# Optimization experiments

Hardware: AMD Instinct MI355X
Metric: run time of the kernel (lower is better)

The kernel has to match this reference:

```python
import jax, jax.numpy as jnp
import numpy as np

INPUT_DIM = 2048
NUM_EXPERTS = 64
TOP_K = 8
BATCH = 16384


def setup_inputs() -> dict:
    key = jax.random.key(0)
    k_x, k_n, k_wg, k_bg, k_wn = jax.random.split(key, 5)
    x = jax.random.normal(k_x, (BATCH, INPUT_DIM), dtype=jnp.float32)
    noise = jax.random.normal(k_n, (BATCH, NUM_EXPERTS), dtype=jnp.float32)
    Wg = jax.random.normal(k_wg, (NUM_EXPERTS, INPUT_DIM), dtype=jnp.float32) * 0.02
    bg = jax.random.normal(k_bg, (NUM_EXPERTS,), dtype=jnp.float32) * 0.02
    Wn = jax.random.normal(k_wn, (NUM_EXPERTS, INPUT_DIM), dtype=jnp.float32) * 0.02
    return {"x": x, "noise": noise, "Wg": Wg, "bg": bg, "Wn": Wn}


def reference(x, noise, Wg, bg, Wn):
    # logits: (B, E)
    logits = jnp.einsum("bd,ed->be", x, Wg) + bg
    noise_stddev = jax.nn.softplus(jnp.einsum("bd,ed->be", x, Wn))
    noisy_logits = logits + noise * noise_stddev

    top_k_values, top_k_indices = jax.lax.top_k(noisy_logits, TOP_K)  # (B, K)
    top_k_weights = jax.nn.softmax(top_k_values, axis=-1)

    # aux losses
    dispatch = jnp.argmax(noisy_logits, axis=-1)            # (B,)
    f = jax.nn.one_hot(dispatch, NUM_EXPERTS, dtype=logits.dtype).mean(axis=0)  # (E,)
    p = jax.nn.softmax(logits, axis=-1).mean(axis=0)        # (E,)
    load_balance_loss = NUM_EXPERTS * jnp.sum(f * p)
    z_loss = jnp.mean(jax.nn.logsumexp(logits, axis=-1) ** 2)

    return top_k_weights, top_k_indices, load_balance_loss, z_loss
```

## Files before the change

### kernel.cpp

```cpp
#include <hip/hip_runtime.h>
#include <math.h>

#define IDIM 2048
#define NE   64
#define TOPK 8
#define NB   16384
#define BM   32
#define BK   64
#define NCH  (IDIM / BK)
#define NQ   4
#define KQ   512
#define NCHQ 8
#define TAU  1e-4f

#define WS_CNT 129
#define WS_LIST 130
#define WSPLIT_BYTE 66560
#define WSPLIT_REQ  (WSPLIT_BYTE + NCH * 32768)
#define PART_BYTE   (WSPLIT_BYTE + NCH * 32768)
#define SPLIT_REQ   (PART_BYTE + (size_t)NQ * NB * 128 * 4)

typedef __attribute__((ext_vector_type(8))) short bf16x8_t;
typedef __attribute__((ext_vector_type(4))) float f32x4_t;

__device__ __forceinline__ float softplusf(float v) {
    return (v > 0.f) ? (v + log1pf(expf(-v))) : log1pf(expf(v));
}
__device__ __forceinline__ double softplus_d(double v) {
    return (v > 0.0) ? (v + log1p(exp(-v))) : log1p(exp(v));
}

__device__ __forceinline__ short f2bf(float f) {
    unsigned u = __float_as_uint(f);
    unsigned r = (u + 0x7FFFu + ((u >> 16) & 1u)) >> 16;
    return (short)r;
}
__device__ __forceinline__ float bf2f(short s) {
    return __uint_as_float(((unsigned)(unsigned short)s) << 16);
}

__global__ void init_ws_kernel(float* ws) {
    int t = threadIdx.x;
    if (t < WS_LIST) ws[t] = 0.0f;
}

__device__ __forceinline__ void split8(const float4 v0, const float4 v1,
                                       bf16x8_t& H, bf16x8_t& L) {
    float fv[8] = {v0.x, v0.y, v0.z, v0.w, v1.x, v1.y, v1.z, v1.w};
    #pragma unroll
    for (int q = 0; q < 8; ++q) {
        short hb = f2bf(fv[q]);
        short lb = f2bf(fv[q] - bf2f(hb));
        H[q] = hb; L[q] = lb;
    }
}

__device__ __forceinline__ void cvt_slot(const float4 v0, const float4 v1,
                                         char* hiP, char* loP, int off) {
    bf16x8_t H, L;
    split8(v0, v1, H, L);
    *(bf16x8_t*)(hiP + off) = H;
    *(bf16x8_t*)(loP + off) = L;
}

__global__ __launch_bounds__(256) void prep_kernel(
    const float* __restrict__ Wg, const float* __restrict__ Wn,
    char* __restrict__ wsW, float* __restrict__ ws)
{
    if (blockIdx.x == 128) {
        if (threadIdx.x < WS_LIST) ws[threadIdx.x] = 0.0f;
        return;
    }
    int g = blockIdx.x * 256 + threadIdx.x;
    int t = g >> 10, i = g & 1023;
    int row = i >> 3, wslot = i & 7;
    int kslot = wslot ^ (row & 7);
    const float* src = (row < 64 ? Wg + (size_t)row * IDIM
                                 : Wn + (size_t)(row - 64) * IDIM) + t * BK + kslot * 8;
    float4 v0 = *(const float4*)src;
    float4 v1 = *(const float4*)(src + 4);
    bf16x8_t H, L;
    split8(v0, v1, H, L);
    char* dst = wsW + (size_t)t * 32768;
    *(bf16x8_t*)(dst + i * 16)         = H;
    *(bf16x8_t*)(dst + 16384 + i * 16) = L;
}

__global__ __launch_bounds__(512, 4) void gemm_quarter_kernel(
    const float* __restrict__ x, const char* __restrict__ wsW,
    float* __restrict__ part)
{
    __shared__ char smem[40960] __attribute__((aligned(16)));
    char* AH = smem;
    char* AL = smem + 4096;
    char* BH = smem + 8192;
    char* BL = smem + 24576;

    const int u   = threadIdx.x;
    const int w   = u >> 6;
    const int l   = u & 63;
    const int lr  = l & 15;
    const int lg4 = l >> 4;
    const int s7  = lr & 7;
    const int q   = blockIdx.x & 3;
    const int row0 = (blockIdx.x >> 2) * BM;
    float* pb = part + (size_t)q * NB * 128;

    const int ar  = (u >> 3) & 31;
    const int ac  = u & 7;
    const int aoff = ar * 128 + (((ac ^ (ar & 7)) & 7) << 4);
    const float* pa = x + (size_t)(row0 + ar) * IDIM + q * KQ + ac * 8;

    f32x4_t acc[2];
    #pragma unroll
    for (int mt = 0; mt < 2; ++mt) {
        f32x4_t z = {0.f, 0.f, 0.f, 0.f};
        acc[mt] = z;
    }

    float4 ra0, ra1;
    int4 w0, w1, w2, w3;

#define QLOADT(tt) { const int k0 = (tt) * BK;                                  \
    if (u < 256) { ra0 = *(const float4*)(pa + k0);                             \
                   ra1 = *(const float4*)(pa + k0 + 4); }                       \
    const char* s_ = wsW + (size_t)(q * NCHQ + (tt)) * 32768 + u * 16;          \
    w0 = *(const int4*)(s_);          w1 = *(const int4*)(s_ + 8192);           \
    w2 = *(const int4*)(s_ + 16384);  w3 = *(const int4*)(s_ + 24576); }

    QLOADT(0);

    for (int t = 0; t < NCHQ; ++t) {
        __syncthreads();
        if (u < 256) cvt_slot(ra0, ra1, AH, AL, aoff);
        *(int4*)(BH + u * 16)        = w0;
        *(int4*)(BH + 8192 + u * 16) = w1;
        *(int4*)(BL + u * 16)        = w2;
        *(int4*)(BL + 8192 + u * 16) = w3;
        if (t + 1 < NCHQ) QLOADT(t + 1);
        __syncthreads();

        #pragma unroll
        for (int ks = 0; ks < 2; ++ks) {
            const int so = (((ks * 4 + lg4) ^ s7) << 4);
            bf16x8_t ah[2], al_[2], bh, bl;
            #pragma unroll
            for (int mt = 0; mt < 2; ++mt) {
                const int o = (mt * 16 + lr) * 128 + so;
                ah[mt]  = *(const bf16x8_t*)(AH + o);
                al_[mt] = *(const bf16x8_t*)(AL + o);
            }
            {
                const int o = (w * 16 + lr) * 128 + so;
                bh = *(const bf16x8_t*)(BH + o);
                bl = *(const bf16x8_t*)(BL + o);
            }
            #pragma unroll
            for (int mt = 0; mt < 2; ++mt) {
                acc[mt] = __builtin_amdgcn_mfma_f32_16x16x32_bf16(ah[mt],  bh, acc[mt], 0, 0, 0);
                acc[mt] = __builtin_amdgcn_mfma_f32_16x16x32_bf16(ah[mt],  bl, acc[mt], 0, 0, 0);
                acc[mt] = __builtin_amdgcn_mfma_f32_16x16x32_bf16(al_[mt], bh, acc[mt], 0, 0, 0);
            }
        }
    }

    #pragma unroll
    for (int mt = 0; mt < 2; ++mt)
        #pragma unroll
        for (int r = 0; r < 4; ++r)
            pb[(size_t)(row0 + mt * 16 + lg4 * 4 + r) * 128 + (w * 16 + lr)] = acc[mt][r];
}

__global__ __launch_bounds__(512) void gating_kernel(
    const float* __restrict__ part,
    const float* __restrict__ noise, const float* __restrict__ bg,
    float* __restrict__ out_w, float* __restrict__ out_i,
    float* __restrict__ ws, int listCap)
{
    __shared__ float sP[NE];
    __shared__ float sF[NE];
    __shared__ float sZ[1];
    const int u = threadIdx.x;
    const int w = u >> 6, l = u & 63;
    const int row0 = blockIdx.x * 32;
    const float* p0 = part;
    const float* p1 = part + (size_t)NB * 128;
    const float* p2 = part + 2 * (size_t)NB * 128;
    const float* p3 = part + 3 * (size_t)NB * 128;

    if (u < NE) { sP[u] = 0.f; sF[u] = 0.f; }
    if (u == 0) sZ[0] = 0.f;
    __syncthreads();

    float pacc = 0.f, zacc = 0.f;
    #pragma unroll 1
    for (int rr = 0; rr < 4; ++rr) {
        const int grow = row0 + w * 4 + rr;
        const size_t b = (size_t)grow * 128;
        float lg   = ((p0[b + l] + p1[b + l]) + (p2[b + l] + p3[b + l])) + bg[l];
        float npre = (p0[b + 64 + l] + p1[b + 64 + l]) + (p2[b + 64 + l] + p3[b + 64 + l]);
        float vcur = fmaf(noise[(size_t)grow * NE + l], softplusf(npre), lg);

        float tkv[9]; int tki[9];
        #pragma unroll
        for (int k = 0; k < 9; ++k) {
            float mv = vcur; int mi = l;
            #pragma unroll
            for (int o = 32; o > 0; o >>= 1) {
                float ov = __shfl_xor(mv, o);
                int   oi = __shfl_xor(mi, o);
                if (ov > mv || (ov == mv && oi < mi)) { mv = ov; mi = oi; }
            }
            tkv[k] = mv; tki[k] = mi;
            if (l == mi) vcur = -1e30f;
        }

        float m0 = tkv[0], s = 0.f, wk[TOPK];
        #pragma unroll
        for (int k = 0; k < TOPK; ++k) { wk[k] = expf(tkv[k] - m0); s += wk[k]; }
        float inv = 1.f / s;
        float myw = 0.f; int myi = 0;
        #pragma unroll
        for (int k = 0; k < TOPK; ++k)
            if (l == k) { myw = wk[k] * inv; myi = tki[k]; }
        if (l < TOPK) {
            out_w[(size_t)grow * TOPK + l] = myw;
            out_i[(size_t)grow * TOPK + l] = (float)myi;
        }

        if (l == 0) {
            atomicAdd(&sF[tki[0]], 1.f);
            float ming = 1e30f;
            #pragma unroll
            for (int k = 0; k < 8; ++k) ming = fminf(ming, tkv[k] - tkv[k + 1]);
            if (ming < TAU) {
                int slot = atomicAdd((int*)&ws[WS_CNT], 1);
                if (slot < listCap) ((int*)ws)[WS_LIST + slot] = grow;
            }
        }

        float rm = lg;
        #pragma unroll
        for (int o = 32; o > 0; o >>= 1) rm = fmaxf(rm, __shfl_xor(rm, o));
        float pe = expf(lg - rm);
        float ssum = pe;
        #pragma unroll
        for (int o = 32; o > 0; o >>= 1) ssum += __shfl_xor(ssum, o);
        pacc += pe / ssum;
        if (l == 0) { float lse = rm + logf(ssum); zacc += lse * lse; }
    }

    atomicAdd(&sP[l], pacc);
    if (l == 0) atomicAdd(sZ, zacc);
    __syncthreads();
    if (u < NE) {
        atomicAdd(&ws[u],      sF[u]);
        atomicAdd(&ws[NE + u], sP[u]);
    }
    if (u == 0) atomicAdd(&ws[2 * NE], sZ[0]);
}

template<bool PRE>
__global__ __launch_bounds__(512, 4) void gate_main_kernel(
    const float* __restrict__ x, const float* __restrict__ noise,
    const float* __restrict__ Wg, const float* __restrict__ bg,
    const float* __restrict__ Wn, const char* __restrict__ wsW,
    float* __restrict__ out_w, float* __restrict__ out_i,
    float* __restrict__ ws, int listCap)
{
    __shared__ char smem[41488] __attribute__((aligned(16)));
    char* AH = smem;
    char* AL = smem + 4096;
    char* BH = smem + 8192;
    char* BL = smem + 24576;
    float* sP = (float*)(smem + 40960);
    float* sF = (float*)(smem + 41216);
    float* sZ = (float*)(smem + 41472);
    float* sL = (float*)smem;

    const int u   = threadIdx.x;
    const int w   = u >> 6;
    const int l   = u & 63;
    const int lr  = l & 15;
    const int lg4 = l >> 4;
    const int s7  = lr & 7;
    const int row0 = blockIdx.x * BM;

    if (u < NE) { sP[u] = 0.f; sF[u] = 0.f; }
    if (u == 0) sZ[0] = 0.f;

    const int ar  = (u >> 3) & 31;
    const int ac  = u & 7;
    const int aoff = ar * 128 + (((ac ^ (ar & 7)) & 7) << 4);
    const float* pa = x + (size_t)(row0 + ar) * IDIM + ac * 8;

    const int br  = u >> 3;
    const float* pg = Wg + (size_t)br * IDIM + ac * 8;
    const float* pn = Wn + (size_t)br * IDIM + ac * 8;
    const int woff = br * 128 + ((ac ^ (br & 7)) << 4);

    f32x4_t acc[2];
    #pragma unroll
    for (int mt = 0; mt < 2; ++mt) {
        f32x4_t z = {0.f, 0.f, 0.f, 0.f};
        acc[mt] = z;
    }

    float4 ra0, ra1;
    int4 w0, w1, w2, w3;
    float4 g0, g1, n0, n1;

#define LOADT(tt) { const int k0 = (tt) * BK;                                   \
    if (u < 256) { ra0 = *(const float4*)(pa + k0);                             \
                   ra1 = *(const float4*)(pa + k0 + 4); }                       \
    if constexpr (PRE) {                                                        \
        const char* s_ = wsW + (size_t)(tt) * 32768 + u * 16;                   \
        w0 = *(const int4*)(s_);          w1 = *(const int4*)(s_ + 8192);       \
        w2 = *(const int4*)(s_ + 16384);  w3 = *(const int4*)(s_ + 24576);      \
    } else {                                                                    \
        g0 = *(const float4*)(pg + k0);   g1 = *(const float4*)(pg + k0 + 4);   \
        n0 = *(const float4*)(pn + k0);   n1 = *(const float4*)(pn + k0 + 4);   \
    } }

    LOADT(0);

    for (int t = 0; t < NCH; ++t) {
        __syncthreads();
        if (u < 256) cvt_slot(ra0, ra1, AH, AL, aoff);
        if constexpr (PRE) {
            *(int4*)(BH + u * 16)        = w0;
            *(int4*)(BH + 8192 + u * 16) = w1;
            *(int4*)(BL + u * 16)        = w2;
            *(int4*)(BL + 8192 + u * 16) = w3;
        } else {
            cvt_slot(g0, g1, BH, BL, woff);
            cvt_slot(n0, n1, BH, BL, woff + 8192);
        }
        if (t + 1 < NCH) LOADT(t + 1);
        __syncthreads();

        #pragma unroll
        for (int ks = 0; ks < 2; ++ks) {
            const int so = (((ks * 4 + lg4) ^ s7) << 4);
            bf16x8_t ah[2], al_[2], bh, bl;
            #pragma unroll
            for (int mt = 0; mt < 2; ++mt) {
                const int o = (mt * 16 + lr) * 128 + so;
                ah[mt]  = *(const bf16x8_t*)(AH + o);
                al_[mt] = *(const bf16x8_t*)(AL + o);
            }
            {
                const int o = (w * 16 + lr) * 128 + so;
                bh = *(const bf16x8_t*)(BH + o);
                bl = *(const bf16x8_t*)(BL + o);
            }
            #pragma unroll
            for (int mt = 0; mt < 2; ++mt) {
                acc[mt] = __builtin_amdgcn_mfma_f32_16x16x32_bf16(ah[mt],  bh, acc[mt], 0, 0, 0);
                acc[mt] = __builtin_amdgcn_mfma_f32_16x16x32_bf16(ah[mt],  bl, acc[mt], 0, 0, 0);
                acc[mt] = __builtin_amdgcn_mfma_f32_16x16x32_bf16(al_[mt], bh, acc[mt], 0, 0, 0);
            }
        }
    }
    __syncthreads();

    #pragma unroll
    for (int mt = 0; mt < 2; ++mt)
        #pragma unroll
        for (int r = 0; r < 4; ++r)
            sL[(mt * 16 + lg4 * 4 + r) * 132 + (w * 16 + lr)] = acc[mt][r];
    __syncthreads();

    float pacc = 0.f, zacc = 0.f;
    #pragma unroll 1
    for (int rr = 0; rr < 4; ++rr) {
        const int r = w * 4 + rr;
        const int grow = row0 + r;
        float lg   = sL[r * 132 + l] + bg[l];
        float npre = sL[r * 132 + 64 + l];
        float vcur = fmaf(noise[(size_t)grow * NE + l], softplusf(npre), lg);

        float tkv[9]; int tki[9];
        #pragma unroll
        for (int k = 0; k < 9; ++k) {
            float mv = vcur; int mi = l;
            #pragma unroll
            for (int o = 32; o > 0; o >>= 1) {
                float ov = __shfl_xor(mv, o);
                int   oi = __shfl_xor(mi, o);
                if (ov > mv || (ov == mv && oi < mi)) { mv = ov; mi = oi; }
            }
            tkv[k] = mv; tki[k] = mi;
            if (l == mi) vcur = -1e30f;
        }

        float m0 = tkv[0], s = 0.f, wk[TOPK];
        #pragma unroll
        for (int k = 0; k < TOPK; ++k) { wk[k] = expf(tkv[k] - m0); s += wk[k]; }
        float inv = 1.f / s;
        float myw = 0.f; int myi = 0;
        #pragma unroll
        for (int k = 0; k < TOPK; ++k)
            if (l == k) { myw = wk[k] * inv; myi = tki[k]; }
        if (l < TOPK) {
            out_w[(size_t)grow * TOPK + l] = myw;
            out_i[(size_t)grow * TOPK + l] = (float)myi;
        }

        if (l == 0) {
            atomicAdd(&sF[tki[0]], 1.f);
            float ming = 1e30f;
            #pragma unroll
            for (int k = 0; k < 8; ++k) ming = fminf(ming, tkv[k] - tkv[k + 1]);
            if (ming < TAU) {
                int slot = atomicAdd((int*)&ws[WS_CNT], 1);
                if (slot < listCap) ((int*)ws)[WS_LIST + slot] = grow;
            }
        }

        float rm = lg;
        #pragma unroll
        for (int o = 32; o > 0; o >>= 1) rm = fmaxf(rm, __shfl_xor(rm, o));
        float pe = expf(lg - rm);
        float ssum = pe;
        #pragma unroll
        for (int o = 32; o > 0; o >>= 1) ssum += __shfl_xor(ssum, o);
        pacc += pe / ssum;
        if (l == 0) { float lse = rm + logf(ssum); zacc += lse * lse; }
    }

    atomicAdd(&sP[l], pacc);
    if (l == 0) atomicAdd(sZ, zacc);
    __syncthreads();
    if (u < NE) {
        atomicAdd(&ws[u],      sF[u]);
        atomicAdd(&ws[NE + u], sP[u]);
    }
    if (u == 0) atomicAdd(&ws[2 * NE], sZ[0]);
}

__global__ __launch_bounds__(1024) void recheck_finalize_kernel(
    const float* __restrict__ x, const float* __restrict__ noise,
    const float* __restrict__ Wg, const float* __restrict__ bg,
    const float* __restrict__ Wn,
    float* __restrict__ out_w, float* __restrict__ out_i, float* __restrict__ out_s,
    const float* __restrict__ ws, int listCap)
{
    __shared__ double sRed[2048];
    const int t = threadIdx.x;

    if (blockIdx.x == 0 && t < 64) {
        float v = (ws[t] / (float)NB) * (ws[NE + t] / (float)NB);
        #pragma unroll
        for (int o = 32; o > 0; o >>= 1) v += __shfl_down(v, o);
        if (t == 0) {
            out_s[0] = (float)NE * v;
            out_s[1] = ws[2 * NE] / (float)NB;
        }
    }

    const int* wsi = (const int*)ws;
    int cnt = wsi[WS_CNT];
    if (cnt > listCap) cnt = listCap;
    if (cnt <= 0) return;

    const int slot = t & 127;
    const int kg   = t >> 7;
    const float* wrb = ((slot < 64) ? (Wg + (size_t)slot * IDIM)
                                    : (Wn + (size_t)(slot - 64) * IDIM)) + kg * 256;

    const int npair = (cnt + 1) >> 1;
    for (int bi = blockIdx.x; bi < npair; bi += gridDim.x) {
        const int i1 = 2 * bi + 1;
        const int r0 = wsi[WS_LIST + 2 * bi];
        const int r1 = wsi[WS_LIST + (i1 < cnt ? i1 : cnt - 1)];
        const float* x0 = x + (size_t)r0 * IDIM + kg * 256;
        const float* x1 = x + (size_t)r1 * IDIM + kg * 256;

        double a0 = 0.0, a1 = 0.0;
        #pragma unroll 4
        for (int k = 0; k < 256; k += 4) {
            float4 wv  = *(const float4*)(wrb + k);
            float4 xv0 = *(const float4*)(x0 + k);
            float4 xv1 = *(const float4*)(x1 + k);
            a0 = fma((double)xv0.x, (double)wv.x, a0);
            a1 = fma((double)xv1.x, (double)wv.x, a1);
            a0 = fma((double)xv0.y, (double)wv.y, a0);
            a1 = fma((double)xv1.y, (double)wv.y, a1);
            a0 = fma((double)xv0.z, (double)wv.z, a0);
            a1 = fma((double)xv1.z, (double)wv.z, a1);
            a0 = fma((double)xv0.w, (double)wv.w, a0);
            a1 = fma((double)xv1.w, (double)wv.w, a1);
        }
        sRed[t * 2]     = a0;
        sRed[t * 2 + 1] = a1;
        __syncthreads();
        if (t < 128) {
            double s0 = 0.0, s1 = 0.0;
            #pragma unroll
            for (int g = 0; g < 8; ++g) {
                s0 += sRed[(g * 128 + t) * 2];
                s1 += sRed[(g * 128 + t) * 2 + 1];
            }
            sRed[t * 2]     = s0;
            sRed[t * 2 + 1] = s1;
        }
        __syncthreads();

        if (t < 64) {
            const int lane = t;
            const double bgl = (double)bg[lane];
            #pragma unroll 1
            for (int i = 0; i < 2; ++i) {
                const int row = i ? r1 : r0;
                double g = sRed[lane * 2 + i];
                double n = sRed[(64 + lane) * 2 + i];
                double lgd = g + bgl;
                double nz = (double)noise[(size_t)row * NE + lane];
                double vcur = fma(nz, softplus_d(n), lgd);

                double tkv[TOPK]; int tki[TOPK];
                #pragma unroll
                for (int k = 0; k < TOPK; ++k) {
                    double mv = vcur; int mi = lane;
                    #pragma unroll
                    for (int o = 32; o > 0; o >>= 1) {
                        double ov = __shfl_xor(mv, o);
                        int    oi = __shfl_xor(mi, o);
                        if (ov > mv || (ov == mv && oi < mi)) { mv = ov; mi = oi; }
                    }
                    tkv[k] = mv; tki[k] = mi;
                    if (lane == mi) vcur = -1e300;
                }
                double m0 = tkv[0], s = 0.0, wk[TOPK];
                #pragma unroll
                for (int k = 0; k < TOPK; ++k) { wk[k] = exp(tkv[k] - m0); s += wk[k]; }
                double inv = 1.0 / s;
                float myw = 0.f; int myi = 0;
                #pragma unroll
                for (int k = 0; k < TOPK; ++k)
                    if (lane == k) { myw = (float)(wk[k] * inv); myi = tki[k]; }
                if (lane < TOPK) {
                    out_w[(size_t)row * TOPK + lane] = myw;
                    out_i[(size_t)row * TOPK + lane] = (float)myi;
                }
            }
        }
        __syncthreads();
    }
}

extern "C" void kernel_launch(void* const* d_in, const int* in_sizes, int n_in,
                              void* d_out, int out_size, void* d_ws, size_t ws_size,
                              hipStream_t stream) {
    const float* x     = (const float*)d_in[0];
    const float* noise = (const float*)d_in[1];
    const float* Wg    = (const float*)d_in[2];
    const float* bg    = (const float*)d_in[3];
    const float* Wn    = (const float*)d_in[4];
    float* out = (float*)d_out;
    float* ws  = (float*)d_ws;
    char*  wsW = (char*)d_ws + WSPLIT_BYTE;

    long cap = (long)(ws_size / 4) - WS_LIST;
    int listCap = (int)(cap < 0 ? 0 : (cap > NB ? NB : cap));
    const bool pre   = ws_size >= (size_t)WSPLIT_REQ;
    const bool split = ws_size >= (size_t)SPLIT_REQ;

    if (split) {
        float* part = (float*)((char*)d_ws + PART_BYTE);
        hipLaunchKernelGGL(prep_kernel, dim3(129), dim3(256), 0, stream, Wg, Wn, wsW, ws);
        hipLaunchKernelGGL(gemm_quarter_kernel, dim3(NQ * NB / BM), dim3(512), 0, stream,
                           x, wsW, part);
        hipLaunchKernelGGL(gating_kernel, dim3(NB / 32), dim3(512), 0, stream,
                           part, noise, bg,
                           out, out + (size_t)NB * TOPK, ws, listCap);
    } else if (pre) {
        hipLaunchKernelGGL(prep_kernel, dim3(129), dim3(256), 0, stream, Wg, Wn, wsW, ws);
        hipLaunchKernelGGL(gate_main_kernel<true>, dim3(NB / BM), dim3(512), 0, stream,
                           x, noise, Wg, bg, Wn, wsW,
                           out, out + (size_t)NB * TOPK, ws, listCap);
    } else {
        hipLaunchKernelGGL(init_ws_kernel, dim3(1), dim3(256), 0, stream, ws);
        hipLaunchKernelGGL(gate_main_kernel<false>, dim3(NB / BM), dim3(512), 0, stream,
                           x, noise, Wg, bg, Wn, wsW,
                           out, out + (size_t)NB * TOPK, ws, listCap);
    }
    hipLaunchKernelGGL(recheck_finalize_kernel, dim3(1024), dim3(1024), 0, stream,
                       x, noise, Wg, bg, Wn,
                       out, out + (size_t)NB * TOPK, out + 2 * (size_t)NB * TOPK,
                       ws, listCap);
}
```

Baseline: 146.6 us.

## Restructure recheck kernel to one row per block with wave-per-slot reduction

The recheck kernel used to process row pairs, with each thread covering a 256-element k-slice for one weight slot and a two-stage LDS reduction. Now each block handles a single flagged row: the x row is held in registers, each wave computes 8 weight slots with a full-row dot product, and partial sums are combined by wave shuffles. Shared memory shrinks and one sync stage is removed. The grid is halved to 512 blocks, which means less parallelism when the flagged list is large, and each row now gets its own pass over the weights.

```diff
diff --git a/kernel.cpp b/kernel.cpp
--- a/kernel.cpp
+++ b/kernel.cpp
@@ -446,7 +446,7 @@
     float* __restrict__ out_w, float* __restrict__ out_i, float* __restrict__ out_s,
     const float* __restrict__ ws, int listCap)
 {
-    __shared__ double sRed[2048];
+    __shared__ double sRed[128];
     const int t = threadIdx.x;
 
     if (blockIdx.x == 0 && t < 64) {
@@ -464,86 +464,71 @@
     if (cnt > listCap) cnt = listCap;
     if (cnt <= 0) return;
 
-    const int slot = t & 127;
-    const int kg   = t >> 7;
-    const float* wrb = ((slot < 64) ? (Wg + (size_t)slot * IDIM)
-                                    : (Wn + (size_t)(slot - 64) * IDIM)) + kg * 256;
-
-    const int npair = (cnt + 1) >> 1;
-    for (int bi = blockIdx.x; bi < npair; bi += gridDim.x) {
-        const int i1 = 2 * bi + 1;
-        const int r0 = wsi[WS_LIST + 2 * bi];
-        const int r1 = wsi[WS_LIST + (i1 < cnt ? i1 : cnt - 1)];
-        const float* x0 = x + (size_t)r0 * IDIM + kg * 256;
-        const float* x1 = x + (size_t)r1 * IDIM + kg * 256;
-
-        double a0 = 0.0, a1 = 0.0;
-        #pragma unroll 4
-        for (int k = 0; k < 256; k += 4) {
-            float4 wv  = *(const float4*)(wrb + k);
-            float4 xv0 = *(const float4*)(x0 + k);
-            float4 xv1 = *(const float4*)(x1 + k);
-            a0 = fma((double)xv0.x, (double)wv.x, a0);
-            a1 = fma((double)xv1.x, (double)wv.x, a1);
-            a0 = fma((double)xv0.y, (double)wv.y, a0);
-            a1 = fma((double)xv1.y, (double)wv.y, a1);
-            a0 = fma((double)xv0.z, (double)wv.z, a0);
-            a1 = fma((double)xv1.z, (double)wv.z, a1);
-            a0 = fma((double)xv0.w, (double)wv.w, a0);
-            a1 = fma((double)xv1.w, (double)wv.w, a1);
-        }
-        sRed[t * 2]     = a0;
-        sRed[t * 2 + 1] = a1;
+    const int wv   = t >> 6;
+    const int lane = t & 63;
+
+    for (int bi = blockIdx.x; bi < cnt; bi += gridDim.x) {
+        const int row = wsi[WS_LIST + bi];
+        const float* xr = x + (size_t)row * IDIM;
+
+        float4 xv[8];
+        #pragma unroll
+        for (int i = 0; i < 8; ++i)
+            xv[i] = *(const float4*)(xr + i * 256 + lane * 4);
+
+        #pragma unroll 1
+        for (int si = 0; si < 8; ++si) {
+            const int s = wv * 8 + si;
+            const float* wr = (s < 64) ? (Wg + (size_t)s * IDIM)
+                                       : (Wn + (size_t)(s - 64) * IDIM);
+            double a = 0.0;
+            #pragma unroll
+            for (int i = 0; i < 8; ++i) {
+                float4 wvv = *(const float4*)(wr + i * 256 + lane * 4);
+                a = fma((double)xv[i].x, (double)wvv.x, a);
+                a = fma((double)xv[i].y, (double)wvv.y, a);
+                a = fma((double)xv[i].z, (double)wvv.z, a);
+                a = fma((double)xv[i].w, (double)wvv.w, a);
+            }
+            #pragma unroll
+            for (int o = 32; o > 0; o >>= 1)
+                a += __shfl_xor(a, o);
+            if (lane == 0) sRed[s] = a;
+        }
         __syncthreads();
-        if (t < 128) {
-            double s0 = 0.0, s1 = 0.0;
-            #pragma unroll
-            for (int g = 0; g < 8; ++g) {
-                s0 += sRed[(g * 128 + t) * 2];
-                s1 += sRed[(g * 128 + t) * 2 + 1];
-            }
-            sRed[t * 2]     = s0;
-            sRed[t * 2 + 1] = s1;
-        }
-        __syncthreads();
 
         if (t < 64) {
-            const int lane = t;
-            const double bgl = (double)bg[lane];
-            #pragma unroll 1
-            for (int i = 0; i < 2; ++i) {
-                const int row = i ? r1 : r0;
-                double g = sRed[lane * 2 + i];
-                double n = sRed[(64 + lane) * 2 + i];
-                double lgd = g + bgl;
-                double nz = (double)noise[(size_t)row * NE + lane];
-                double vcur = fma(nz, softplus_d(n), lgd);
-
-                double tkv[TOPK]; int tki[TOPK];
+            const int l64 = t;
+            double g = sRed[l64];
+            double n = sRed[64 + l64];
+            double lgd = g + (double)bg[l64];
+            double nz = (double)noise[(size_t)row * NE + l64];
+            double vcur = fma(nz, softplus_d(n), lgd);
+
+            double tkv[TOPK]; int tki[TOPK];
+            #pragma unroll
+            for (int k = 0; k < TOPK; ++k) {
+                double mv = vcur; int mi = l64;
                 #pragma unroll
-                for (int k = 0; k < TOPK; ++k) {
-                    double mv = vcur; int mi = lane;
-                    #pragma unroll
-                    for (int o = 32; o > 0; o >>= 1) {
-                        double ov = __shfl_xor(mv, o);
-                        int    oi = __shfl_xor(mi, o);
-                        if (ov > mv || (ov == mv && oi < mi)) { mv = ov; mi = oi; }
-                    }
-                    tkv[k] = mv; tki[k] = mi;
-                    if (lane == mi) vcur = -1e300;
+                for (int o = 32; o > 0; o >>= 1) {
+                    double ov = __shfl_xor(mv, o);
+                    int    oi = __shfl_xor(mi, o);
+                    if (ov > mv || (ov == mv && oi < mi)) { mv = ov; mi = oi; }
                 }
-                double m0 = tkv[0], s = 0.0, wk[TOPK];
-                #pragma unroll
-                for (int k = 0; k < TOPK; ++k) { wk[k] = exp(tkv[k] - m0); s += wk[k]; }
-                double inv = 1.0 / s;
-                float myw = 0.f; int myi = 0;
-                #pragma unroll
-                for (int k = 0; k < TOPK; ++k)
-                    if (lane == k) { myw = (float)(wk[k] * inv); myi = tki[k]; }
-                if (lane < TOPK) {
-                    out_w[(size_t)row * TOPK + lane] = myw;
-                    out_i[(size_t)row * TOPK + lane] = (float)myi;
-                }
+                tkv[k] = mv; tki[k] = mi;
+                if (l64 == mi) vcur = -1e300;
+            }
+            double m0 = tkv[0], s = 0.0, wk[TOPK];
+            #pragma unroll
+            for (int k = 0; k < TOPK; ++k) { wk[k] = exp(tkv[k] - m0); s += wk[k]; }
+            double inv = 1.0 / s;
+            float myw = 0.f; int myi = 0;
+            #pragma unroll
+            for (int k = 0; k < TOPK; ++k)
+                if (l64 == k) { myw = (float)(wk[k] * inv); myi = tki[k]; }
+            if (l64 < TOPK) {
+                out_w[(size_t)row * TOPK + l64] = myw;
+                out_i[(size_t)row * TOPK + l64] = (float)myi;
             }
         }
         __syncthreads();
@@ -586,7 +571,7 @@
                            x, noise, Wg, bg, Wn, wsW,
                            out, out + (size_t)NB * TOPK, ws, listCap);
     }
-    hipLaunchKernelGGL(recheck_finalize_kernel, dim3(1024), dim3(1024), 0, stream,
+    hipLaunchKernelGGL(recheck_finalize_kernel, dim3(512), dim3(1024), 0, stream,
                        x, noise, Wg, bg, Wn,
                        out, out + (size_t)NB * TOPK, out + 2 * (size_t)NB * TOPK,
                        ws, listCap);
```

New measurement: 118.0 us, median of 2. 1.24x faster.
